# Performance work log

Measured on AMD Instinct MI355X. Metric: run time of the kernel, lower is better.

The kernel has to match this reference:

```python
import jax, jax.numpy as jnp
import numpy as np

BN_EPS = 1e-5

def _mlp(h, w1, b1, w2, b2):
    return jax.nn.relu(h @ w1 + b1) @ w2 + b2

def _segment_mean(data, seg, num_segments):
    s = jax.ops.segment_sum(data, seg, num_segments=num_segments)
    c = jax.ops.segment_sum(jnp.ones((data.shape[0],), data.dtype), seg, num_segments=num_segments)
    return s / jnp.maximum(c, 1.0)[:, None]

def _lin_init(k, fan_in, fan_out):
    k1, k2 = jax.random.split(k)
    s = 1.0 / float(np.sqrt(fan_in))
    w = jax.random.uniform(k1, (fan_in, fan_out), jnp.float32, -s, s)
    b = jax.random.uniform(k2, (fan_out,), jnp.float32, -s, s)
    return w, b

def setup_inputs() -> dict:
    key = jax.random.key(0)
    ks = jax.random.split(key, 16)
    N, E, B = 100000, 1600000, 256
    d1, d2, d3, d5, nc = 3, 50, 15, 10, 6
    x = jax.random.normal(ks[0], (N, d1), jnp.float32)
    edge_index = jax.random.randint(ks[1], (2, E), 0, N)
    edge_attr = jax.random.normal(ks[2], (E, d1), jnp.float32)
    u = jax.random.normal(ks[3], (B, 1), jnp.float32)
    batch = jnp.sort(jax.random.randint(ks[4], (N,), 0, B))
    ew1, eb1 = _lin_init(ks[5], d1 * 3, d2)
    ew2, eb2 = _lin_init(ks[6], d2, d3)
    nw1, nb1 = _lin_init(ks[7], d1 * 6, d2)
    nw2, nb2 = _lin_init(ks[8], d2, d3)
    gw1, gb1 = _lin_init(ks[9], d3 + 1, d2)
    gw2, gb2 = _lin_init(ks[10], d2, d3)
    fc1_w, fc1_b = _lin_init(ks[11], d3, d5)
    bn_g = jnp.ones((d5,), jnp.float32)
    bn_b = jnp.zeros((d5,), jnp.float32)
    fc2_w, fc2_b = _lin_init(ks[12], d5, nc)
    return dict(x=x, edge_index=edge_index, edge_attr=edge_attr, u=u, batch=batch,
                ew1=ew1, eb1=eb1, ew2=ew2, eb2=eb2,
                nw1=nw1, nb1=nb1, nw2=nw2, nb2=nb2,
                gw1=gw1, gb1=gb1, gw2=gw2, gb2=gb2,
                fc1_w=fc1_w, fc1_b=fc1_b, bn_g=bn_g, bn_b=bn_b,
                fc2_w=fc2_w, fc2_b=fc2_b)

def reference(x, edge_index, edge_attr, u, batch,
              ew1, eb1, ew2, eb2, nw1, nb1, nw2, nb2,
              gw1, gb1, gw2, gb2, fc1_w, fc1_b, bn_g, bn_b, fc2_w, fc2_b):
    N = x.shape[0]
    B = u.shape[0]
    row, col = edge_index[0], edge_index[1]
    # edge update: cat([x[row], x[col], edge_attr]) -> MLP  => [E, d3]
    e2 = _mlp(jnp.concatenate([x[row], x[col], edge_attr], axis=1), ew1, eb1, ew2, eb2)
    # node update: cat([x[col], e2]) -> MLP -> scatter_mean over row  => [N, d3]
    h = _mlp(jnp.concatenate([x[col], e2], axis=1), nw1, nb1, nw2, nb2)
    x2 = _segment_mean(h, row, N)
    # global update: cat([u, mean_per_graph(x2)]) -> MLP  => [B, d3]
    u2 = _mlp(jnp.concatenate([u, _segment_mean(x2, batch, B)], axis=1), gw1, gb1, gw2, gb2)
    # readout: relu(cat nodes + globals), mean-pool per graph (u2 rows join their graph)
    z = jax.nn.relu(jnp.concatenate([x2, u2], axis=0))  # dropout off (eval mode)
    seg = jnp.concatenate([batch, jnp.arange(B, dtype=batch.dtype)])
    g = _segment_mean(z, seg, B)  # [B, d3]
    h1 = g @ fc1_w + fc1_b
    # BatchNorm1d in eval mode with default running stats (mean=0, var=1)
    h1 = jax.nn.relu(h1 * (bn_g / jnp.sqrt(1.0 + BN_EPS)) + bn_b)
    return jax.nn.log_softmax(h1 @ fc2_w + fc2_b, axis=1)
```

## Files before the change

### kernel.cpp

```cpp
#include <hip/hip_runtime.h>
#include <math.h>

#define D1 3
#define D2 50
#define D3 15
#define D5 10
#define NC 6
#define SCAN_B 256

typedef _Float16 h2 __attribute__((ext_vector_type(2)));
typedef __fp16   fp16x2 __attribute__((ext_vector_type(2)));

__device__ __forceinline__ float fdot2(h2 a, h2 b, float c) {
#if __has_builtin(__builtin_amdgcn_fdot2)
    return __builtin_amdgcn_fdot2(a, b, c, false);
#else
    return c + (float)a[0] * (float)b[0] + (float)a[1] * (float)b[1];
#endif
}

__device__ __forceinline__ h2 pkrtz(float a, float b) {
#if __has_builtin(__builtin_amdgcn_cvt_pkrtz)
    fp16x2 r = __builtin_amdgcn_cvt_pkrtz(a, b);
    return __builtin_bit_cast(h2, r);
#else
    h2 v; v[0] = (_Float16)a; v[1] = (_Float16)b; return v;
#endif
}

__global__ __launch_bounds__(256) void prep_weights_kernel(
    const float* __restrict__ ew1, const float* __restrict__ nw1,
    const float* __restrict__ ew2, const float* __restrict__ nw2,
    h2* __restrict__ ew1pk, h2* __restrict__ nw1pk,
    h2* __restrict__ ew2pk, h2* __restrict__ nw2pk)
{
    int t = threadIdx.x;
    for (int i = t; i < D2 * 5; i += 256) {
        int j = i / 5, p = i - 5 * j;
        float a = ew1[(2 * p) * D2 + j];
        float b = (2 * p + 1 < 9) ? ew1[(2 * p + 1) * D2 + j] : 0.0f;
        h2 v; v[0] = (_Float16)a; v[1] = (_Float16)b;
        ew1pk[i] = v;
    }
    for (int i = t; i < D2 * 9; i += 256) {
        int j = i / 9, p = i - 9 * j;
        float a = nw1[(2 * p) * D2 + j];
        float b = nw1[(2 * p + 1) * D2 + j];
        h2 v; v[0] = (_Float16)a; v[1] = (_Float16)b;
        nw1pk[i] = v;
    }
    for (int i = t; i < D3 * 25; i += 256) {
        int m = i / 25, k = i - 25 * m;
        float a = ew2[(2 * k) * D3 + m];
        float b = ew2[(2 * k + 1) * D3 + m];
        h2 v; v[0] = (_Float16)a; v[1] = (_Float16)b;
        ew2pk[i] = v;
        float c = nw2[(2 * k) * D3 + m];
        float d = nw2[(2 * k + 1) * D3 + m];
        h2 w; w[0] = (_Float16)c; w[1] = (_Float16)d;
        nw2pk[i] = w;
    }
}

__global__ __launch_bounds__(256) void deg_rank_kernel(
    const int* __restrict__ ei, int* __restrict__ deg, int* __restrict__ rank, int E)
{
    int e = blockIdx.x * blockDim.x + threadIdx.x;
    if (e >= E) return;
    int r = ei[e];
    rank[e] = atomicAdd(&deg[r], 1);
}

__global__ __launch_bounds__(SCAN_B) void scan1_kernel(
    const int* __restrict__ deg, int* __restrict__ base, int* __restrict__ bsum, int N)
{
    __shared__ int sm[SCAN_B];
    int i = blockIdx.x * SCAN_B + threadIdx.x;
    int v = (i < N) ? deg[i] : 0;
    sm[threadIdx.x] = v;
    __syncthreads();
    #pragma unroll
    for (int s = 1; s < SCAN_B; s <<= 1) {
        int t = (threadIdx.x >= s) ? sm[threadIdx.x - s] : 0;
        __syncthreads();
        sm[threadIdx.x] += t;
        __syncthreads();
    }
    if (i < N) base[i] = sm[threadIdx.x] - v;
    if (threadIdx.x == SCAN_B - 1) bsum[blockIdx.x] = sm[threadIdx.x];
}

__global__ __launch_bounds__(1024) void scan2_kernel(int* __restrict__ bsum, int nb)
{
    __shared__ int sm[1024];
    int v = ((int)threadIdx.x < nb) ? bsum[threadIdx.x] : 0;
    sm[threadIdx.x] = v;
    __syncthreads();
    #pragma unroll
    for (int s = 1; s < 1024; s <<= 1) {
        int t = (threadIdx.x >= s) ? sm[threadIdx.x - s] : 0;
        __syncthreads();
        sm[threadIdx.x] += t;
        __syncthreads();
    }
    if ((int)threadIdx.x < nb) bsum[threadIdx.x] = sm[threadIdx.x] - v;
}

__global__ __launch_bounds__(SCAN_B) void scan3_kernel(
    int* __restrict__ base, const int* __restrict__ bsum, int N)
{
    int i = blockIdx.x * SCAN_B + threadIdx.x;
    if (i < N) base[i] += bsum[blockIdx.x];
}

__global__ __launch_bounds__(256, 4) void edge_mlp_fused_kernel(
    const float* __restrict__ x,
    const int*   __restrict__ ei,
    const float* __restrict__ ea,
    const h2* __restrict__ ew1pk, const float* __restrict__ eb1,
    const h2* __restrict__ ew2pk, const float* __restrict__ eb2,
    const h2* __restrict__ nw1pk, const float* __restrict__ nb1,
    const h2* __restrict__ nw2pk, const float* __restrict__ nb2,
    const int* __restrict__ base, const int* __restrict__ rank,
    unsigned int* __restrict__ hbuf16,
    int E)
{
    int e = blockIdx.x * blockDim.x + threadIdx.x;
    if (e >= E) return;

    int r = ei[e];
    int c = ei[E + e];
    int slot = base[r] + rank[e];

    float in9[9];
    in9[0] = x[3 * r + 0];
    in9[1] = x[3 * r + 1];
    in9[2] = x[3 * r + 2];
    in9[3] = x[3 * c + 0];
    in9[4] = x[3 * c + 1];
    in9[5] = x[3 * c + 2];
    in9[6] = ea[3 * e + 0];
    in9[7] = ea[3 * e + 1];
    in9[8] = ea[3 * e + 2];

    h2 inpk[5];
    inpk[0] = pkrtz(in9[0], in9[1]);
    inpk[1] = pkrtz(in9[2], in9[3]);
    inpk[2] = pkrtz(in9[4], in9[5]);
    inpk[3] = pkrtz(in9[6], in9[7]);
    inpk[4] = pkrtz(in9[8], 0.0f);

    h2 hpk[25];
    #pragma unroll
    for (int jj = 0; jj < 25; ++jj) {
        float a0 = eb1[2 * jj];
        float a1 = eb1[2 * jj + 1];
        #pragma unroll
        for (int p = 0; p < 5; ++p) {
            a0 = fdot2(inpk[p], ew1pk[(2 * jj) * 5 + p], a0);
            a1 = fdot2(inpk[p], ew1pk[(2 * jj + 1) * 5 + p], a1);
        }
        hpk[jj] = pkrtz(fmaxf(a0, 0.0f), fmaxf(a1, 0.0f));
    }

    float e2v[D3];
    #pragma unroll
    for (int m = 0; m < D3; ++m) {
        float a = eb2[m];
        #pragma unroll
        for (int k = 0; k < 25; ++k) a = fdot2(hpk[k], ew2pk[m * 25 + k], a);
        e2v[m] = a;
    }

    h2 vpk[9];
    vpk[0] = pkrtz(in9[3], in9[4]);
    vpk[1] = pkrtz(in9[5], e2v[0]);
    #pragma unroll
    for (int p = 2; p < 9; ++p) vpk[p] = pkrtz(e2v[2 * p - 3], e2v[2 * p - 2]);

    h2 h2pk[25];
    #pragma unroll
    for (int jj = 0; jj < 25; ++jj) {
        float a0 = nb1[2 * jj];
        float a1 = nb1[2 * jj + 1];
        #pragma unroll
        for (int p = 0; p < 9; ++p) {
            a0 = fdot2(vpk[p], nw1pk[(2 * jj) * 9 + p], a0);
            a1 = fdot2(vpk[p], nw1pk[(2 * jj + 1) * 9 + p], a1);
        }
        h2pk[jj] = pkrtz(fmaxf(a0, 0.0f), fmaxf(a1, 0.0f));
    }

    float acc[D3 + 1];
    #pragma unroll
    for (int m = 0; m < D3; ++m) {
        float a = nb2[m];
        #pragma unroll
        for (int k = 0; k < 25; ++k) a = fdot2(h2pk[k], nw2pk[m * 25 + k], a);
        acc[m] = a;
    }
    acc[D3] = 0.0f;

    union { h2 h[8]; uint4 u[2]; } outp;
    #pragma unroll
    for (int p = 0; p < 8; ++p) outp.h[p] = pkrtz(acc[2 * p], acc[2 * p + 1]);

    uint4* dst = (uint4*)(hbuf16 + (size_t)slot * 8);
    dst[0] = outp.u[0];
    dst[1] = outp.u[1];
}

__global__ __launch_bounds__(256) void gather_kernel(
    const unsigned int* __restrict__ hbuf16, const int* __restrict__ deg,
    const int* __restrict__ base, float* __restrict__ x2, int N)
{
    int idx = blockIdx.x * blockDim.x + threadIdx.x;
    if (idx >= N * 8) return;
    int n = idx >> 3;
    int p = idx & 7;
    int b = base[n];
    int d = deg[n];
    float s0 = 0.0f, s1 = 0.0f;
    for (int k = 0; k < d; ++k) {
        unsigned int w = hbuf16[(size_t)(b + k) * 8 + p];
        h2 v = __builtin_bit_cast(h2, w);
        s0 += (float)v[0];
        s1 += (float)v[1];
    }
    float inv = 1.0f / fmaxf((float)d, 1.0f);
    x2[(size_t)n * D3 + 2 * p] = s0 * inv;
    if (p < 7) x2[(size_t)n * D3 + 2 * p + 1] = s1 * inv;
}

__global__ __launch_bounds__(256) void graph_sum_x2_kernel(
    const float* __restrict__ x2,
    const int* __restrict__ batch, int N,
    float* __restrict__ bx, float* __restrict__ brelu, float* __restrict__ ncnt)
{
    int b = blockIdx.x;

    int lo = 0, hi = N;
    while (lo < hi) { int m = (lo + hi) >> 1; if (batch[m] < b) lo = m + 1; else hi = m; }
    int start = lo;
    hi = N;
    while (lo < hi) { int m = (lo + hi) >> 1; if (batch[m] < b + 1) lo = m + 1; else hi = m; }
    int end = lo;

    float sx[D3], sr[D3];
    #pragma unroll
    for (int j = 0; j < D3; ++j) { sx[j] = 0.0f; sr[j] = 0.0f; }

    for (int i = start + (int)threadIdx.x; i < end; i += (int)blockDim.x) {
        #pragma unroll
        for (int j = 0; j < D3; ++j) {
            float v = x2[(size_t)i * D3 + j];
            sx[j] += v;
            sr[j] += fmaxf(v, 0.0f);
        }
    }

    #pragma unroll
    for (int j = 0; j < D3; ++j) {
        #pragma unroll
        for (int s = 32; s > 0; s >>= 1) {
            sx[j] += __shfl_down(sx[j], s);
            sr[j] += __shfl_down(sr[j], s);
        }
    }

    __shared__ float sm[4][2 * D3];
    int lane = threadIdx.x & 63, wid = threadIdx.x >> 6;
    if (lane == 0) {
        #pragma unroll
        for (int j = 0; j < D3; ++j) { sm[wid][j] = sx[j]; sm[wid][D3 + j] = sr[j]; }
    }
    __syncthreads();
    if (threadIdx.x < 2 * D3) {
        float v = sm[0][threadIdx.x] + sm[1][threadIdx.x] + sm[2][threadIdx.x] + sm[3][threadIdx.x];
        if (threadIdx.x < D3) bx[b * D3 + threadIdx.x] = v;
        else                  brelu[b * D3 + (threadIdx.x - D3)] = v;
    }
    if (threadIdx.x == 0) ncnt[b] = (float)(end - start);
}

__global__ __launch_bounds__(256) void final_kernel(
    const float* __restrict__ u,
    const float* __restrict__ gw1, const float* __restrict__ gb1,
    const float* __restrict__ gw2, const float* __restrict__ gb2,
    const float* __restrict__ fc1w, const float* __restrict__ fc1b,
    const float* __restrict__ bng, const float* __restrict__ bnb,
    const float* __restrict__ fc2w, const float* __restrict__ fc2b,
    const float* __restrict__ bx, const float* __restrict__ brelu,
    const float* __restrict__ ncnt,
    float* __restrict__ out, int B)
{
    int t = blockIdx.x * blockDim.x + threadIdx.x;
    if (t >= B) return;

    float nct = ncnt[t];
    float inv = 1.0f / fmaxf(nct, 1.0f);

    float in16[16];
    in16[0] = u[t];
    #pragma unroll
    for (int j = 0; j < D3; ++j) in16[1 + j] = bx[t * D3 + j] * inv;

    float gh[D2];
    #pragma unroll
    for (int j = 0; j < D2; ++j) {
        float a = gb1[j];
        #pragma unroll
        for (int k = 0; k < 16; ++k) a = fmaf(in16[k], gw1[k * D2 + j], a);
        gh[j] = fmaxf(a, 0.0f);
    }

    float g[D3];
    #pragma unroll
    for (int j = 0; j < D3; ++j) {
        float a = gb2[j];
        #pragma unroll
        for (int k = 0; k < D2; ++k) a = fmaf(gh[k], gw2[k * D3 + j], a);
        g[j] = (brelu[t * D3 + j] + fmaxf(a, 0.0f)) / (nct + 1.0f);
    }

    const float bnscale = 1.0f / sqrtf(1.0f + 1e-5f);
    float h1[D5];
    #pragma unroll
    for (int i = 0; i < D5; ++i) {
        float a = fc1b[i];
        #pragma unroll
        for (int k = 0; k < D3; ++k) a = fmaf(g[k], fc1w[k * D5 + i], a);
        h1[i] = fmaxf(a * (bng[i] * bnscale) + bnb[i], 0.0f);
    }

    float o[NC];
    #pragma unroll
    for (int j = 0; j < NC; ++j) {
        float a = fc2b[j];
        #pragma unroll
        for (int k = 0; k < D5; ++k) a = fmaf(h1[k], fc2w[k * NC + j], a);
        o[j] = a;
    }
    float m = o[0];
    #pragma unroll
    for (int j = 1; j < NC; ++j) m = fmaxf(m, o[j]);
    float ssum = 0.0f;
    #pragma unroll
    for (int j = 0; j < NC; ++j) ssum += expf(o[j] - m);
    float lse = m + logf(ssum);
    #pragma unroll
    for (int j = 0; j < NC; ++j) out[t * NC + j] = o[j] - lse;
}

__global__ __launch_bounds__(256) void edge_node_atomic_kernel(
    const float* __restrict__ x,
    const int*   __restrict__ ei,
    const float* __restrict__ ea,
    const float* __restrict__ ew1, const float* __restrict__ eb1,
    const float* __restrict__ ew2, const float* __restrict__ eb2,
    const float* __restrict__ nw1, const float* __restrict__ nb1,
    const float* __restrict__ nw2, const float* __restrict__ nb2,
    float* __restrict__ x2sum, float* __restrict__ cnt,
    int E)
{
    int e = blockIdx.x * blockDim.x + threadIdx.x;
    if (e >= E) return;
    int r = ei[e];
    int c = ei[E + e];
    float in9[9];
    in9[0] = x[3 * r + 0]; in9[1] = x[3 * r + 1]; in9[2] = x[3 * r + 2];
    float xc0 = x[3 * c + 0], xc1 = x[3 * c + 1], xc2 = x[3 * c + 2];
    in9[3] = xc0; in9[4] = xc1; in9[5] = xc2;
    in9[6] = ea[3 * e + 0]; in9[7] = ea[3 * e + 1]; in9[8] = ea[3 * e + 2];
    float h[D2];
    #pragma unroll
    for (int j = 0; j < D2; ++j) {
        float a = eb1[j];
        #pragma unroll
        for (int k = 0; k < 9; ++k) a = fmaf(in9[k], ew1[k * D2 + j], a);
        h[j] = fmaxf(a, 0.0f);
    }
    float e2[D3];
    #pragma unroll
    for (int j = 0; j < D3; ++j) {
        float a = eb2[j];
        #pragma unroll
        for (int k = 0; k < D2; ++k) a = fmaf(h[k], ew2[k * D3 + j], a);
        e2[j] = a;
    }
    float h2v[D2];
    #pragma unroll
    for (int j = 0; j < D2; ++j) {
        float a = nb1[j];
        a = fmaf(xc0, nw1[0 * D2 + j], a);
        a = fmaf(xc1, nw1[1 * D2 + j], a);
        a = fmaf(xc2, nw1[2 * D2 + j], a);
        #pragma unroll
        for (int k = 0; k < D3; ++k) a = fmaf(e2[k], nw1[(3 + k) * D2 + j], a);
        h2v[j] = fmaxf(a, 0.0f);
    }
    float* dst = x2sum + (size_t)r * D3;
    #pragma unroll
    for (int j = 0; j < D3; ++j) {
        float a = nb2[j];
        #pragma unroll
        for (int k = 0; k < D2; ++k) a = fmaf(h2v[k], nw2[k * D3 + j], a);
        atomicAdd(&dst[j], a);
    }
    atomicAdd(&cnt[r], 1.0f);
}

__global__ __launch_bounds__(256) void graph_sum_atomic_kernel(
    const float* __restrict__ x2sum, const float* __restrict__ cnt,
    const int* __restrict__ batch, int N,
    float* __restrict__ bx, float* __restrict__ brelu, float* __restrict__ ncnt)
{
    int b = blockIdx.x;
    int lo = 0, hi = N;
    while (lo < hi) { int m = (lo + hi) >> 1; if (batch[m] < b) lo = m + 1; else hi = m; }
    int start = lo;
    hi = N;
    while (lo < hi) { int m = (lo + hi) >> 1; if (batch[m] < b + 1) lo = m + 1; else hi = m; }
    int end = lo;
    float sx[D3], sr[D3];
    #pragma unroll
    for (int j = 0; j < D3; ++j) { sx[j] = 0.0f; sr[j] = 0.0f; }
    for (int i = start + (int)threadIdx.x; i < end; i += (int)blockDim.x) {
        float inv = 1.0f / fmaxf(cnt[i], 1.0f);
        #pragma unroll
        for (int j = 0; j < D3; ++j) {
            float v = x2sum[(size_t)i * D3 + j] * inv;
            sx[j] += v;
            sr[j] += fmaxf(v, 0.0f);
        }
    }
    #pragma unroll
    for (int j = 0; j < D3; ++j) {
        #pragma unroll
        for (int s = 32; s > 0; s >>= 1) {
            sx[j] += __shfl_down(sx[j], s);
            sr[j] += __shfl_down(sr[j], s);
        }
    }
    __shared__ float sm[4][2 * D3];
    int lane = threadIdx.x & 63, wid = threadIdx.x >> 6;
    if (lane == 0) {
        #pragma unroll
        for (int j = 0; j < D3; ++j) { sm[wid][j] = sx[j]; sm[wid][D3 + j] = sr[j]; }
    }
    __syncthreads();
    if (threadIdx.x < 2 * D3) {
        float v = sm[0][threadIdx.x] + sm[1][threadIdx.x] + sm[2][threadIdx.x] + sm[3][threadIdx.x];
        if (threadIdx.x < D3) bx[b * D3 + threadIdx.x] = v;
        else                  brelu[b * D3 + (threadIdx.x - D3)] = v;
    }
    if (threadIdx.x == 0) ncnt[b] = (float)(end - start);
}

extern "C" void kernel_launch(void* const* d_in, const int* in_sizes, int n_in,
                              void* d_out, int out_size, void* d_ws, size_t ws_size,
                              hipStream_t stream) {
    const float* x     = (const float*)d_in[0];
    const int*   ei    = (const int*)  d_in[1];
    const float* ea    = (const float*)d_in[2];
    const float* u     = (const float*)d_in[3];
    const int*   batch = (const int*)  d_in[4];
    const float* ew1 = (const float*)d_in[5];
    const float* eb1 = (const float*)d_in[6];
    const float* ew2 = (const float*)d_in[7];
    const float* eb2 = (const float*)d_in[8];
    const float* nw1 = (const float*)d_in[9];
    const float* nb1 = (const float*)d_in[10];
    const float* nw2 = (const float*)d_in[11];
    const float* nb2 = (const float*)d_in[12];
    const float* gw1 = (const float*)d_in[13];
    const float* gb1 = (const float*)d_in[14];
    const float* gw2 = (const float*)d_in[15];
    const float* gb2 = (const float*)d_in[16];
    const float* fc1w = (const float*)d_in[17];
    const float* fc1b = (const float*)d_in[18];
    const float* bng  = (const float*)d_in[19];
    const float* bnb  = (const float*)d_in[20];
    const float* fc2w = (const float*)d_in[21];
    const float* fc2b = (const float*)d_in[22];

    int N = in_sizes[0] / 3;
    int E = in_sizes[2] / 3;
    int B = in_sizes[3];
    float* out = (float*)d_out;

    int nsb = (N + SCAN_B - 1) / SCAN_B;

    const size_t WPK = 2048;

    size_t need = sizeof(h2) * WPK
                + sizeof(unsigned int) * (size_t)E * 8
                + sizeof(int) * ((size_t)N + (size_t)E + (size_t)N + 1024)
                + sizeof(float) * ((size_t)N * D3 + 2u * B * D3 + B);

    if (ws_size >= need && nsb <= 1024) {
        char* p = (char*)d_ws;
        h2* ew1pk = (h2*)p;
        h2* nw1pk = ew1pk + 250;
        h2* ew2pk = nw1pk + 450;
        h2* nw2pk = ew2pk + 375;
        p += sizeof(h2) * WPK;
        unsigned int* hbuf16 = (unsigned int*)p;  p += sizeof(unsigned int) * (size_t)E * 8;
        int* deg  = (int*)p;            p += sizeof(int) * (size_t)N;
        int* rank = (int*)p;            p += sizeof(int) * (size_t)E;
        int* base = (int*)p;            p += sizeof(int) * (size_t)N;
        int* bsum = (int*)p;            p += sizeof(int) * 1024;
        float* x2   = (float*)p;        p += sizeof(float) * (size_t)N * D3;
        float* bx    = (float*)p;       p += sizeof(float) * (size_t)B * D3;
        float* brelu = (float*)p;       p += sizeof(float) * (size_t)B * D3;
        float* ncnt  = (float*)p;

        hipMemsetAsync(deg, 0, sizeof(int) * (size_t)N, stream);

        prep_weights_kernel<<<1, 256, 0, stream>>>(ew1, nw1, ew2, nw2,
                                                   ew1pk, nw1pk, ew2pk, nw2pk);

        int eb = (E + 255) / 256;
        deg_rank_kernel<<<eb, 256, 0, stream>>>(ei, deg, rank, E);

        scan1_kernel<<<nsb, SCAN_B, 0, stream>>>(deg, base, bsum, N);
        scan2_kernel<<<1, 1024, 0, stream>>>(bsum, nsb);
        scan3_kernel<<<nsb, SCAN_B, 0, stream>>>(base, bsum, N);

        edge_mlp_fused_kernel<<<eb, 256, 0, stream>>>(
            x, ei, ea, ew1pk, eb1, ew2pk, eb2, nw1pk, nb1, nw2pk, nb2,
            base, rank, hbuf16, E);

        int gtb = (N * 8 + 255) / 256;
        gather_kernel<<<gtb, 256, 0, stream>>>(hbuf16, deg, base, x2, N);

        graph_sum_x2_kernel<<<B, 256, 0, stream>>>(x2, batch, N, bx, brelu, ncnt);

        int fb = (B + 255) / 256;
        final_kernel<<<fb, 256, 0, stream>>>(
            u, gw1, gb1, gw2, gb2, fc1w, fc1b, bng, bnb, fc2w, fc2b,
            bx, brelu, ncnt, out, B);
    } else {
        float* x2sum = (float*)d_ws;
        float* cnt   = x2sum + (size_t)N * D3;
        float* bx    = cnt + N;
        float* brelu = bx + (size_t)B * D3;
        float* ncnt  = brelu + (size_t)B * D3;

        hipMemsetAsync(x2sum, 0, sizeof(float) * ((size_t)N * D3 + N), stream);

        int eb = (E + 255) / 256;
        edge_node_atomic_kernel<<<eb, 256, 0, stream>>>(
            x, ei, ea, ew1, eb1, ew2, eb2, nw1, nb1, nw2, nb2, x2sum, cnt, E);

        graph_sum_atomic_kernel<<<B, 256, 0, stream>>>(x2sum, cnt, batch, N, bx, brelu, ncnt);

        int fb = (B + 255) / 256;
        final_kernel<<<fb, 256, 0, stream>>>(
            u, gw1, gb1, gw2, gb2, fc1w, fc1b, bng, bnb, fc2w, fc2b,
            bx, brelu, ncnt, out, B);
    }
}
```

Baseline: 228.6 us.

## Fuse gather, graph pooling and final MLP into one per-graph tail kernel

Folds the weight-packing kernel into the degree/rank kernel (block 0 also packs weights), doubles the scan block size, and replaces the separate gather, graph-sum and final kernels with a single tail kernel launched one block per graph. In the tail kernel each thread reads one node's CSR segment of fp16 edge outputs as 16-byte vectors, forms the node mean, and accumulates graph sums directly, then the block runs the global MLP, readout and log-softmax. This removes the x2 intermediate buffer and two launches. In exchange, parallelism for the gather drops from N*8 threads to 256 blocks of 256 threads, about 390 nodes per block, so each thread serially walks about 16 edges per node and may be latency bound.

After: 209.5 us. 8.3% less time.

```diff
diff --git a/kernel.cpp b/kernel.cpp
--- a/kernel.cpp
+++ b/kernel.cpp
@@ -6,7 +6,7 @@
 #define D3 15
 #define D5 10
 #define NC 6
-#define SCAN_B 256
+#define SCAN_B 512
 
 typedef _Float16 h2 __attribute__((ext_vector_type(2)));
 typedef __fp16   fp16x2 __attribute__((ext_vector_type(2)));
@@ -28,47 +28,46 @@
 #endif
 }
 
-__global__ __launch_bounds__(256) void prep_weights_kernel(
+__global__ __launch_bounds__(256) void deg_rank_prep_kernel(
+    const int* __restrict__ ei, int* __restrict__ deg, int* __restrict__ rank, int E,
     const float* __restrict__ ew1, const float* __restrict__ nw1,
     const float* __restrict__ ew2, const float* __restrict__ nw2,
     h2* __restrict__ ew1pk, h2* __restrict__ nw1pk,
     h2* __restrict__ ew2pk, h2* __restrict__ nw2pk)
 {
-    int t = threadIdx.x;
-    for (int i = t; i < D2 * 5; i += 256) {
-        int j = i / 5, p = i - 5 * j;
-        float a = ew1[(2 * p) * D2 + j];
-        float b = (2 * p + 1 < 9) ? ew1[(2 * p + 1) * D2 + j] : 0.0f;
-        h2 v; v[0] = (_Float16)a; v[1] = (_Float16)b;
-        ew1pk[i] = v;
-    }
-    for (int i = t; i < D2 * 9; i += 256) {
-        int j = i / 9, p = i - 9 * j;
-        float a = nw1[(2 * p) * D2 + j];
-        float b = nw1[(2 * p + 1) * D2 + j];
-        h2 v; v[0] = (_Float16)a; v[1] = (_Float16)b;
-        nw1pk[i] = v;
-    }
-    for (int i = t; i < D3 * 25; i += 256) {
-        int m = i / 25, k = i - 25 * m;
-        float a = ew2[(2 * k) * D3 + m];
-        float b = ew2[(2 * k + 1) * D3 + m];
-        h2 v; v[0] = (_Float16)a; v[1] = (_Float16)b;
-        ew2pk[i] = v;
-        float c = nw2[(2 * k) * D3 + m];
-        float d = nw2[(2 * k + 1) * D3 + m];
-        h2 w; w[0] = (_Float16)c; w[1] = (_Float16)d;
-        nw2pk[i] = w;
-    }
-}
-
-__global__ __launch_bounds__(256) void deg_rank_kernel(
-    const int* __restrict__ ei, int* __restrict__ deg, int* __restrict__ rank, int E)
-{
     int e = blockIdx.x * blockDim.x + threadIdx.x;
-    if (e >= E) return;
-    int r = ei[e];
-    rank[e] = atomicAdd(&deg[r], 1);
+    if (e < E) {
+        int r = ei[e];
+        rank[e] = atomicAdd(&deg[r], 1);
+    }
+    if (blockIdx.x == 0) {
+        int t = threadIdx.x;
+        for (int i = t; i < D2 * 5; i += 256) {
+            int j = i / 5, p = i - 5 * j;
+            float a = ew1[(2 * p) * D2 + j];
+            float b = (2 * p + 1 < 9) ? ew1[(2 * p + 1) * D2 + j] : 0.0f;
+            h2 v; v[0] = (_Float16)a; v[1] = (_Float16)b;
+            ew1pk[i] = v;
+        }
+        for (int i = t; i < D2 * 9; i += 256) {
+            int j = i / 9, p = i - 9 * j;
+            float a = nw1[(2 * p) * D2 + j];
+            float b = nw1[(2 * p + 1) * D2 + j];
+            h2 v; v[0] = (_Float16)a; v[1] = (_Float16)b;
+            nw1pk[i] = v;
+        }
+        for (int i = t; i < D3 * 25; i += 256) {
+            int m = i / 25, k = i - 25 * m;
+            float a = ew2[(2 * k) * D3 + m];
+            float b = ew2[(2 * k + 1) * D3 + m];
+            h2 v; v[0] = (_Float16)a; v[1] = (_Float16)b;
+            ew2pk[i] = v;
+            float c = nw2[(2 * k) * D3 + m];
+            float d = nw2[(2 * k + 1) * D3 + m];
+            h2 w; w[0] = (_Float16)c; w[1] = (_Float16)d;
+            nw2pk[i] = w;
+        }
+    }
 }
 
 __global__ __launch_bounds__(SCAN_B) void scan1_kernel(
@@ -81,7 +80,7 @@
     __syncthreads();
     #pragma unroll
     for (int s = 1; s < SCAN_B; s <<= 1) {
-        int t = (threadIdx.x >= s) ? sm[threadIdx.x - s] : 0;
+        int t = (threadIdx.x >= (unsigned)s) ? sm[threadIdx.x - s] : 0;
         __syncthreads();
         sm[threadIdx.x] += t;
         __syncthreads();
@@ -98,7 +97,7 @@
     __syncthreads();
     #pragma unroll
     for (int s = 1; s < 1024; s <<= 1) {
-        int t = (threadIdx.x >= s) ? sm[threadIdx.x - s] : 0;
+        int t = (threadIdx.x >= (unsigned)s) ? sm[threadIdx.x - s] : 0;
         __syncthreads();
         sm[threadIdx.x] += t;
         __syncthreads();
@@ -210,34 +209,20 @@
     dst[1] = outp.u[1];
 }
 
-__global__ __launch_bounds__(256) void gather_kernel(
-    const unsigned int* __restrict__ hbuf16, const int* __restrict__ deg,
-    const int* __restrict__ base, float* __restrict__ x2, int N)
-{
-    int idx = blockIdx.x * blockDim.x + threadIdx.x;
-    if (idx >= N * 8) return;
-    int n = idx >> 3;
-    int p = idx & 7;
-    int b = base[n];
-    int d = deg[n];
-    float s0 = 0.0f, s1 = 0.0f;
-    for (int k = 0; k < d; ++k) {
-        unsigned int w = hbuf16[(size_t)(b + k) * 8 + p];
-        h2 v = __builtin_bit_cast(h2, w);
-        s0 += (float)v[0];
-        s1 += (float)v[1];
-    }
-    float inv = 1.0f / fmaxf((float)d, 1.0f);
-    x2[(size_t)n * D3 + 2 * p] = s0 * inv;
-    if (p < 7) x2[(size_t)n * D3 + 2 * p + 1] = s1 * inv;
-}
-
-__global__ __launch_bounds__(256) void graph_sum_x2_kernel(
-    const float* __restrict__ x2,
+__global__ __launch_bounds__(256) void tail_kernel(
+    const unsigned int* __restrict__ hbuf16,
+    const int* __restrict__ deg, const int* __restrict__ base,
     const int* __restrict__ batch, int N,
-    float* __restrict__ bx, float* __restrict__ brelu, float* __restrict__ ncnt)
+    const float* __restrict__ u,
+    const float* __restrict__ gw1, const float* __restrict__ gb1,
+    const float* __restrict__ gw2, const float* __restrict__ gb2,
+    const float* __restrict__ fc1w, const float* __restrict__ fc1b,
+    const float* __restrict__ bng, const float* __restrict__ bnb,
+    const float* __restrict__ fc2w, const float* __restrict__ fc2b,
+    float* __restrict__ out)
 {
     int b = blockIdx.x;
+    int tid = threadIdx.x;
 
     int lo = 0, hi = N;
     while (lo < hi) { int m = (lo + hi) >> 1; if (batch[m] < b) lo = m + 1; else hi = m; }
@@ -250,10 +235,28 @@
     #pragma unroll
     for (int j = 0; j < D3; ++j) { sx[j] = 0.0f; sr[j] = 0.0f; }
 
-    for (int i = start + (int)threadIdx.x; i < end; i += (int)blockDim.x) {
+    for (int i = start + tid; i < end; i += 256) {
+        int bs = deg ? base[i] : 0;
+        int d  = deg[i];
+        float acc[16];
+        #pragma unroll
+        for (int j = 0; j < 16; ++j) acc[j] = 0.0f;
+        const uint4* ptr = (const uint4*)(hbuf16 + (size_t)bs * 8);
+        for (int k = 0; k < d; ++k) {
+            uint4 w0 = ptr[2 * k];
+            uint4 w1 = ptr[2 * k + 1];
+            unsigned int ws[8] = {w0.x, w0.y, w0.z, w0.w, w1.x, w1.y, w1.z, w1.w};
+            #pragma unroll
+            for (int p = 0; p < 8; ++p) {
+                h2 v = __builtin_bit_cast(h2, ws[p]);
+                acc[2 * p]     += (float)v[0];
+                acc[2 * p + 1] += (float)v[1];
+            }
+        }
+        float inv = 1.0f / fmaxf((float)d, 1.0f);
         #pragma unroll
         for (int j = 0; j < D3; ++j) {
-            float v = x2[(size_t)i * D3 + j];
+            float v = acc[j] * inv;
             sx[j] += v;
             sr[j] += fmaxf(v, 0.0f);
         }
@@ -268,6 +271,168 @@
         }
     }
 
+    __shared__ float sm[4][2 * D3];
+    __shared__ float s_red[2 * D3];
+    __shared__ float s_in16[16];
+    __shared__ float s_gh[D2];
+    __shared__ float s_g[D3];
+    __shared__ float s_h1[D5];
+
+    int lane = tid & 63, wid = tid >> 6;
+    if (lane == 0) {
+        #pragma unroll
+        for (int j = 0; j < D3; ++j) { sm[wid][j] = sx[j]; sm[wid][D3 + j] = sr[j]; }
+    }
+    __syncthreads();
+
+    float nct = (float)(end - start);
+
+    if (tid < 2 * D3) {
+        s_red[tid] = sm[0][tid] + sm[1][tid] + sm[2][tid] + sm[3][tid];
+    }
+    __syncthreads();
+
+    if (tid < 16) {
+        s_in16[tid] = (tid == 0) ? u[b] : s_red[tid - 1] / fmaxf(nct, 1.0f);
+    }
+    __syncthreads();
+
+    if (tid < D2) {
+        float a = gb1[tid];
+        #pragma unroll
+        for (int k = 0; k < 16; ++k) a = fmaf(s_in16[k], gw1[k * D2 + tid], a);
+        s_gh[tid] = fmaxf(a, 0.0f);
+    }
+    __syncthreads();
+
+    if (tid < D3) {
+        float a = gb2[tid];
+        #pragma unroll
+        for (int k = 0; k < D2; ++k) a = fmaf(s_gh[k], gw2[k * D3 + tid], a);
+        s_g[tid] = (s_red[D3 + tid] + fmaxf(a, 0.0f)) / (nct + 1.0f);
+    }
+    __syncthreads();
+
+    if (tid < D5) {
+        const float bnscale = 1.0f / sqrtf(1.0f + 1e-5f);
+        float a = fc1b[tid];
+        #pragma unroll
+        for (int k = 0; k < D3; ++k) a = fmaf(s_g[k], fc1w[k * D5 + tid], a);
+        s_h1[tid] = fmaxf(a * (bng[tid] * bnscale) + bnb[tid], 0.0f);
+    }
+    __syncthreads();
+
+    if (tid == 0) {
+        float o[NC];
+        #pragma unroll
+        for (int j = 0; j < NC; ++j) {
+            float a = fc2b[j];
+            #pragma unroll
+            for (int k = 0; k < D5; ++k) a = fmaf(s_h1[k], fc2w[k * NC + j], a);
+            o[j] = a;
+        }
+        float m = o[0];
+        #pragma unroll
+        for (int j = 1; j < NC; ++j) m = fmaxf(m, o[j]);
+        float ssum = 0.0f;
+        #pragma unroll
+        for (int j = 0; j < NC; ++j) ssum += expf(o[j] - m);
+        float lse = m + logf(ssum);
+        #pragma unroll
+        for (int j = 0; j < NC; ++j) out[b * NC + j] = o[j] - lse;
+    }
+}
+
+__global__ __launch_bounds__(256) void edge_node_atomic_kernel(
+    const float* __restrict__ x,
+    const int*   __restrict__ ei,
+    const float* __restrict__ ea,
+    const float* __restrict__ ew1, const float* __restrict__ eb1,
+    const float* __restrict__ ew2, const float* __restrict__ eb2,
+    const float* __restrict__ nw1, const float* __restrict__ nb1,
+    const float* __restrict__ nw2, const float* __restrict__ nb2,
+    float* __restrict__ x2sum, float* __restrict__ cnt,
+    int E)
+{
+    int e = blockIdx.x * blockDim.x + threadIdx.x;
+    if (e >= E) return;
+    int r = ei[e];
+    int c = ei[E + e];
+    float in9[9];
+    in9[0] = x[3 * r + 0]; in9[1] = x[3 * r + 1]; in9[2] = x[3 * r + 2];
+    float xc0 = x[3 * c + 0], xc1 = x[3 * c + 1], xc2 = x[3 * c + 2];
+    in9[3] = xc0; in9[4] = xc1; in9[5] = xc2;
+    in9[6] = ea[3 * e + 0]; in9[7] = ea[3 * e + 1]; in9[8] = ea[3 * e + 2];
+    float h[D2];
+    #pragma unroll
+    for (int j = 0; j < D2; ++j) {
+        float a = eb1[j];
+        #pragma unroll
+        for (int k = 0; k < 9; ++k) a = fmaf(in9[k], ew1[k * D2 + j], a);
+        h[j] = fmaxf(a, 0.0f);
+    }
+    float e2[D3];
+    #pragma unroll
+    for (int j = 0; j < D3; ++j) {
+        float a = eb2[j];
+        #pragma unroll
+        for (int k = 0; k < D2; ++k) a = fmaf(h[k], ew2[k * D3 + j], a);
+        e2[j] = a;
+    }
+    float h2v[D2];
+    #pragma unroll
+    for (int j = 0; j < D2; ++j) {
+        float a = nb1[j];
+        a = fmaf(xc0, nw1[0 * D2 + j], a);
+        a = fmaf(xc1, nw1[1 * D2 + j], a);
+        a = fmaf(xc2, nw1[2 * D2 + j], a);
+        #pragma unroll
+        for (int k = 0; k < D3; ++k) a = fmaf(e2[k], nw1[(3 + k) * D2 + j], a);
+        h2v[j] = fmaxf(a, 0.0f);
+    }
+    float* dst = x2sum + (size_t)r * D3;
+    #pragma unroll
+    for (int j = 0; j < D3; ++j) {
+        float a = nb2[j];
+        #pragma unroll
+        for (int k = 0; k < D2; ++k) a = fmaf(h2v[k], nw2[k * D3 + j], a);
+        atomicAdd(&dst[j], a);
+    }
+    atomicAdd(&cnt[r], 1.0f);
+}
+
+__global__ __launch_bounds__(256) void graph_sum_atomic_kernel(
+    const float* __restrict__ x2sum, const float* __restrict__ cnt,
+    const int* __restrict__ batch, int N,
+    float* __restrict__ bx, float* __restrict__ brelu, float* __restrict__ ncnt)
+{
+    int b = blockIdx.x;
+    int lo = 0, hi = N;
+    while (lo < hi) { int m = (lo + hi) >> 1; if (batch[m] < b) lo = m + 1; else hi = m; }
+    int start = lo;
+    hi = N;
+    while (lo < hi) { int m = (lo + hi) >> 1; if (batch[m] < b + 1) lo = m + 1; else hi = m; }
+    int end = lo;
+    float sx[D3], sr[D3];
+    #pragma unroll
+    for (int j = 0; j < D3; ++j) { sx[j] = 0.0f; sr[j] = 0.0f; }
+    for (int i = start + (int)threadIdx.x; i < end; i += (int)blockDim.x) {
+        float inv = 1.0f / fmaxf(cnt[i], 1.0f);
+        #pragma unroll
+        for (int j = 0; j < D3; ++j) {
+            float v = x2sum[(size_t)i * D3 + j] * inv;
+            sx[j] += v;
+            sr[j] += fmaxf(v, 0.0f);
+        }
+    }
+    #pragma unroll
+    for (int j = 0; j < D3; ++j) {
+        #pragma unroll
+        for (int s = 32; s > 0; s >>= 1) {
+            sx[j] += __shfl_down(sx[j], s);
+            sr[j] += __shfl_down(sr[j], s);
+        }
+    }
     __shared__ float sm[4][2 * D3];
     int lane = threadIdx.x & 63, wid = threadIdx.x >> 6;
     if (lane == 0) {
@@ -350,111 +515,6 @@
     float lse = m + logf(ssum);
     #pragma unroll
     for (int j = 0; j < NC; ++j) out[t * NC + j] = o[j] - lse;
-}
-
-__global__ __launch_bounds__(256) void edge_node_atomic_kernel(
-    const float* __restrict__ x,
-    const int*   __restrict__ ei,
-    const float* __restrict__ ea,
-    const float* __restrict__ ew1, const float* __restrict__ eb1,
-    const float* __restrict__ ew2, const float* __restrict__ eb2,
-    const float* __restrict__ nw1, const float* __restrict__ nb1,
-    const float* __restrict__ nw2, const float* __restrict__ nb2,
-    float* __restrict__ x2sum, float* __restrict__ cnt,
-    int E)
-{
-    int e = blockIdx.x * blockDim.x + threadIdx.x;
-    if (e >= E) return;
-    int r = ei[e];
-    int c = ei[E + e];
-    float in9[9];
-    in9[0] = x[3 * r + 0]; in9[1] = x[3 * r + 1]; in9[2] = x[3 * r + 2];
-    float xc0 = x[3 * c + 0], xc1 = x[3 * c + 1], xc2 = x[3 * c + 2];
-    in9[3] = xc0; in9[4] = xc1; in9[5] = xc2;
-    in9[6] = ea[3 * e + 0]; in9[7] = ea[3 * e + 1]; in9[8] = ea[3 * e + 2];
-    float h[D2];
-    #pragma unroll
-    for (int j = 0; j < D2; ++j) {
-        float a = eb1[j];
-        #pragma unroll
-        for (int k = 0; k < 9; ++k) a = fmaf(in9[k], ew1[k * D2 + j], a);
-        h[j] = fmaxf(a, 0.0f);
-    }
-    float e2[D3];
-    #pragma unroll
-    for (int j = 0; j < D3; ++j) {
-        float a = eb2[j];
-        #pragma unroll
-        for (int k = 0; k < D2; ++k) a = fmaf(h[k], ew2[k * D3 + j], a);
-        e2[j] = a;
-    }
-    float h2v[D2];
-    #pragma unroll
-    for (int j = 0; j < D2; ++j) {
-        float a = nb1[j];
-        a = fmaf(xc0, nw1[0 * D2 + j], a);
-        a = fmaf(xc1, nw1[1 * D2 + j], a);
-        a = fmaf(xc2, nw1[2 * D2 + j], a);
-        #pragma unroll
-        for (int k = 0; k < D3; ++k) a = fmaf(e2[k], nw1[(3 + k) * D2 + j], a);
-        h2v[j] = fmaxf(a, 0.0f);
-    }
-    float* dst = x2sum + (size_t)r * D3;
-    #pragma unroll
-    for (int j = 0; j < D3; ++j) {
-        float a = nb2[j];
-        #pragma unroll
-        for (int k = 0; k < D2; ++k) a = fmaf(h2v[k], nw2[k * D3 + j], a);
-        atomicAdd(&dst[j], a);
-    }
-    atomicAdd(&cnt[r], 1.0f);
-}
-
-__global__ __launch_bounds__(256) void graph_sum_atomic_kernel(
-    const float* __restrict__ x2sum, const float* __restrict__ cnt,
-    const int* __restrict__ batch, int N,
-    float* __restrict__ bx, float* __restrict__ brelu, float* __restrict__ ncnt)
-{
-    int b = blockIdx.x;
-    int lo = 0, hi = N;
-    while (lo < hi) { int m = (lo + hi) >> 1; if (batch[m] < b) lo = m + 1; else hi = m; }
-    int start = lo;
-    hi = N;
-    while (lo < hi) { int m = (lo + hi) >> 1; if (batch[m] < b + 1) lo = m + 1; else hi = m; }
-    int end = lo;
-    float sx[D3], sr[D3];
-    #pragma unroll
-    for (int j = 0; j < D3; ++j) { sx[j] = 0.0f; sr[j] = 0.0f; }
-    for (int i = start + (int)threadIdx.x; i < end; i += (int)blockDim.x) {
-        float inv = 1.0f / fmaxf(cnt[i], 1.0f);
-        #pragma unroll
-        for (int j = 0; j < D3; ++j) {
-            float v = x2sum[(size_t)i * D3 + j] * inv;
-            sx[j] += v;
-            sr[j] += fmaxf(v, 0.0f);
-        }
-    }
-    #pragma unroll
-    for (int j = 0; j < D3; ++j) {
-        #pragma unroll
-        for (int s = 32; s > 0; s >>= 1) {
-            sx[j] += __shfl_down(sx[j], s);
-            sr[j] += __shfl_down(sr[j], s);
-        }
-    }
-    __shared__ float sm[4][2 * D3];
-    int lane = threadIdx.x & 63, wid = threadIdx.x >> 6;
-    if (lane == 0) {
-        #pragma unroll
-        for (int j = 0; j < D3; ++j) { sm[wid][j] = sx[j]; sm[wid][D3 + j] = sr[j]; }
-    }
-    __syncthreads();
-    if (threadIdx.x < 2 * D3) {
-        float v = sm[0][threadIdx.x] + sm[1][threadIdx.x] + sm[2][threadIdx.x] + sm[3][threadIdx.x];
-        if (threadIdx.x < D3) bx[b * D3 + threadIdx.x] = v;
-        else                  brelu[b * D3 + (threadIdx.x - D3)] = v;
-    }
-    if (threadIdx.x == 0) ncnt[b] = (float)(end - start);
 }
 
 extern "C" void kernel_launch(void* const* d_in, const int* in_sizes, int n_in,
@@ -495,8 +555,7 @@
 
     size_t need = sizeof(h2) * WPK
                 + sizeof(unsigned int) * (size_t)E * 8
-                + sizeof(int) * ((size_t)N + (size_t)E + (size_t)N + 1024)
-                + sizeof(float) * ((size_t)N * D3 + 2u * B * D3 + B);
+                + sizeof(int) * ((size_t)N + (size_t)E + (size_t)N + 1024);
 
     if (ws_size >= need && nsb <= 1024) {
         char* p = (char*)d_ws;
@@ -510,18 +569,12 @@
         int* rank = (int*)p;            p += sizeof(int) * (size_t)E;
         int* base = (int*)p;            p += sizeof(int) * (size_t)N;
         int* bsum = (int*)p;            p += sizeof(int) * 1024;
-        float* x2   = (float*)p;        p += sizeof(float) * (size_t)N * D3;
-        float* bx    = (float*)p;       p += sizeof(float) * (size_t)B * D3;
-        float* brelu = (float*)p;       p += sizeof(float) * (size_t)B * D3;
-        float* ncnt  = (float*)p;
 
         hipMemsetAsync(deg, 0, sizeof(int) * (size_t)N, stream);
 
-        prep_weights_kernel<<<1, 256, 0, stream>>>(ew1, nw1, ew2, nw2,
-                                                   ew1pk, nw1pk, ew2pk, nw2pk);
-
         int eb = (E + 255) / 256;
-        deg_rank_kernel<<<eb, 256, 0, stream>>>(ei, deg, rank, E);
+        deg_rank_prep_kernel<<<eb, 256, 0, stream>>>(
+            ei, deg, rank, E, ew1, nw1, ew2, nw2, ew1pk, nw1pk, ew2pk, nw2pk);
 
         scan1_kernel<<<nsb, SCAN_B, 0, stream>>>(deg, base, bsum, N);
         scan2_kernel<<<1, 1024, 0, stream>>>(bsum, nsb);
@@ -531,15 +584,9 @@
             x, ei, ea, ew1pk, eb1, ew2pk, eb2, nw1pk, nb1, nw2pk, nb2,
             base, rank, hbuf16, E);
 
-        int gtb = (N * 8 + 255) / 256;
-        gather_kernel<<<gtb, 256, 0, stream>>>(hbuf16, deg, base, x2, N);
-
-        graph_sum_x2_kernel<<<B, 256, 0, stream>>>(x2, batch, N, bx, brelu, ncnt);
-
-        int fb = (B + 255) / 256;
-        final_kernel<<<fb, 256, 0, stream>>>(
-            u, gw1, gb1, gw2, gb2, fc1w, fc1b, bng, bnb, fc2w, fc2b,
-            bx, brelu, ncnt, out, B);
+        tail_kernel<<<B, 256, 0, stream>>>(
+            hbuf16, deg, base, batch, N,
+            u, gw1, gb1, gw2, gb2, fc1w, fc1b, bng, bnb, fc2w, fc2b, out);
     } else {
         float* x2sum = (float*)d_ws;
         float* cnt   = x2sum + (size_t)N * D3;
```
